# Performance work log

Measured on AMD Instinct MI355X. Metric: run time of the kernel, lower is better.

The kernel has to match this reference:

```python
import jax, jax.numpy as jnp
import numpy as np

VOCAB, E, H, B, T = 32000, 256, 512, 64, 512
PAD = VOCAB - 1


def setup_inputs() -> dict:
    key = jax.random.key(0)
    ks = jax.random.split(key, 9)
    s_ih = 1.0 / np.sqrt(H)
    inp = {
        "x": jax.random.randint(ks[0], (B, T), 0, VOCAB, dtype=jnp.int64 if jax.config.jax_enable_x64 else jnp.int32),
        "length": jax.random.randint(ks[1], (B, 1), 1, T + 1, dtype=jnp.int32),
        "embed_table": (jax.random.normal(ks[2], (VOCAB, E), dtype=jnp.float32)).at[PAD].set(0.0),
        "W_ih": jax.random.uniform(ks[3], (4 * H, E), jnp.float32, -s_ih, s_ih),
        "W_hh": jax.random.uniform(ks[4], (4 * H, H), jnp.float32, -s_ih, s_ih),
        "b_ih": jax.random.uniform(ks[5], (4 * H,), jnp.float32, -s_ih, s_ih),
        "b_hh": jax.random.uniform(ks[6], (4 * H,), jnp.float32, -s_ih, s_ih),
        "W_cls": jax.random.uniform(ks[7], (2, H), jnp.float32, -s_ih, s_ih),
        "b_cls": jax.random.uniform(ks[8], (2,), jnp.float32, -s_ih, s_ih),
    }
    return inp


def _lstm(xg, W_hh):
    # xg: [T, B, 4H] precomputed input-side gate activations; PyTorch gate order i,f,g,o
    Bn = xg.shape[1]
    h0 = jnp.zeros((Bn, H), xg.dtype)
    c0 = jnp.zeros((Bn, H), xg.dtype)

    def step(carry, g_in):
        h, c = carry
        g = g_in + h @ W_hh.T
        i, f, gg, o = jnp.split(g, 4, axis=-1)
        c = jax.nn.sigmoid(f) * c + jax.nn.sigmoid(i) * jnp.tanh(gg)
        h = jax.nn.sigmoid(o) * jnp.tanh(c)
        return (h, c), h

    _, hs = jax.lax.scan(step, (h0, c0), xg)
    return hs  # [T, B, H]


def reference(x, length, embed_table, W_ih, W_hh, b_ih, b_hh, W_cls, b_cls):
    emb_tab = embed_table.at[PAD].set(0.0)  # padding_idx row is zero
    we = emb_tab[x]  # [B, T, E]
    xg = jnp.einsum("bte,ge->btg", we, W_ih) + b_ih + b_hh  # [B, T, 4H]
    hs = _lstm(jnp.swapaxes(xg, 0, 1), W_hh)  # [T, B, H]
    hs = jnp.swapaxes(hs, 0, 1)  # [B, T, H]
    # ragged max-pool over valid timesteps
    mask = jnp.arange(T)[None, :] < length  # [B, T]
    neg = jnp.finfo(hs.dtype).min
    feature = jnp.max(jnp.where(mask[:, :, None], hs, neg), axis=1)  # [B, H]
    return feature @ W_cls.T + b_cls
```

## Files before the change

kernel.cpp:

```cpp
#include <hip/hip_runtime.h>
#include <hip/hip_bf16.h>

#define EN 256
#define HN 512
#define BN 64
#define TN 512
#define NBLK 64
#define KCAT 1280
#define NBUF 8
#define SLOTB 65536

typedef __attribute__((ext_vector_type(8))) short short8;
typedef __attribute__((ext_vector_type(4))) short short4v;
typedef __attribute__((ext_vector_type(4))) float f32x4;

#define SCOPE __HIP_MEMORY_SCOPE_AGENT
#define MFMA(A, B, C) __builtin_amdgcn_mfma_f32_16x16x32_bf16((A), (B), (C), 0, 0, 0)

__device__ inline short bf_of(float f) {
  __hip_bfloat16 h = __float2bfloat16(f);
  return *reinterpret_cast<short*>(&h);
}
__device__ inline float f_of_bf(short s) {
  __hip_bfloat16 h = *reinterpret_cast<__hip_bfloat16*>(&s);
  return __bfloat162float(h);
}

__global__ __launch_bounds__(256) void zero_kernel(unsigned* hb_u32,
                                                   unsigned* flags) {
  int idx = blockIdx.x * 256 + threadIdx.x;
  if (idx < SLOTB / 4)
    __hip_atomic_store(&hb_u32[idx], 0u, __ATOMIC_RELAXED, SCOPE);
  if (idx < NBLK)
    __hip_atomic_store(&flags[idx], 0u, __ATOMIC_RELAXED, SCOPE);
}

__global__ __launch_bounds__(256) void gather_kernel(
    short* __restrict__ weB, const int* __restrict__ x,
    const float* __restrict__ emb) {
  const int t = blockIdx.x;
  const int tid = threadIdx.x;
  const int b = tid >> 2, q = tid & 3;
  const int row = x[b * TN + t];
  const float4* src = (const float4*)(emb + (size_t)row * EN + q * 64);
  short* dst = weB + ((size_t)(t * 64 + b)) * EN + q * 64;
#pragma unroll
  for (int i = 0; i < 16; i++) {
    float4 v = src[i];
    short4v o = { bf_of(v.x), bf_of(v.y), bf_of(v.z), bf_of(v.w) };
    *(short4v*)(dst + i * 4) = o;
  }
}

__global__ __launch_bounds__(256) void prep_w_kernel(
    short* __restrict__ Wall, const float* __restrict__ Wih,
    const float* __restrict__ Whh) {
  int idx = blockIdx.x * 256 + threadIdx.x;
  int grow = idx / KCAT, kc = idx - grow * KCAT;
  float v;
  if (kc < 256) {
    v = Wih[(size_t)grow * EN + kc];
  } else if (kc < 768) {
    v = Whh[(size_t)grow * HN + (kc - 256)];
  } else {
    float f = Whh[(size_t)grow * HN + (kc - 768)];
    v = f - f_of_bf(bf_of(f));
  }
  Wall[idx] = bf_of(v);
}

__device__ __forceinline__ void poll_flags(const unsigned* flags,
                                           unsigned want, int l) {
  bool done = false;
  while (true) {
    if (!done) {
      unsigned v = __hip_atomic_load(&flags[l], __ATOMIC_RELAXED, SCOPE);
      done = (v >= want);
    }
    if (__all(done ? 1 : 0)) break;
    __builtin_amdgcn_s_sleep(1);
  }
  asm volatile("" ::: "memory");
}

#define HLOAD16_ISSUE                                                       \
  asm volatile(                                                             \
    "global_load_dwordx4 %0,  %16, off sc1\n\t"                             \
    "global_load_dwordx4 %1,  %16, off offset:1024 sc1\n\t"                 \
    "global_load_dwordx4 %2,  %16, off offset:2048 sc1\n\t"                 \
    "global_load_dwordx4 %3,  %16, off offset:3072 sc1\n\t"                 \
    "global_load_dwordx4 %4,  %17, off sc1\n\t"                             \
    "global_load_dwordx4 %5,  %17, off offset:1024 sc1\n\t"                 \
    "global_load_dwordx4 %6,  %17, off offset:2048 sc1\n\t"                 \
    "global_load_dwordx4 %7,  %17, off offset:3072 sc1\n\t"                 \
    "global_load_dwordx4 %8,  %18, off sc1\n\t"                             \
    "global_load_dwordx4 %9,  %18, off offset:1024 sc1\n\t"                 \
    "global_load_dwordx4 %10, %18, off offset:2048 sc1\n\t"                 \
    "global_load_dwordx4 %11, %18, off offset:3072 sc1\n\t"                 \
    "global_load_dwordx4 %12, %19, off sc1\n\t"                             \
    "global_load_dwordx4 %13, %19, off offset:1024 sc1\n\t"                 \
    "global_load_dwordx4 %14, %19, off offset:2048 sc1\n\t"                 \
    "global_load_dwordx4 %15, %19, off offset:3072 sc1"                     \
    : "=&v"(hv0), "=&v"(hv1), "=&v"(hv2),  "=&v"(hv3),                      \
      "=&v"(hv4), "=&v"(hv5), "=&v"(hv6),  "=&v"(hv7),                      \
      "=&v"(hv8), "=&v"(hv9), "=&v"(hv10), "=&v"(hv11),                     \
      "=&v"(hv12), "=&v"(hv13), "=&v"(hv14), "=&v"(hv15)                    \
    : "v"(hb0), "v"(hb1), "v"(hb2), "v"(hb3) : "memory")

#define WAIT_HALF                                                           \
  do {                                                                      \
    asm volatile("s_waitcnt vmcnt(8)"                                       \
                 : "+v"(hv0), "+v"(hv1), "+v"(hv2), "+v"(hv3),              \
                   "+v"(hv4), "+v"(hv5), "+v"(hv6), "+v"(hv7)               \
                 :: "memory");                                              \
    __builtin_amdgcn_sched_barrier(0);                                      \
  } while (0)

#define WAIT_ALL                                                            \
  do {                                                                      \
    asm volatile("s_waitcnt vmcnt(0)"                                       \
                 : "+v"(hv8), "+v"(hv9), "+v"(hv10), "+v"(hv11),            \
                   "+v"(hv12), "+v"(hv13), "+v"(hv14), "+v"(hv15)           \
                 :: "memory");                                              \
    __builtin_amdgcn_sched_barrier(0);                                      \
  } while (0)

__global__ __launch_bounds__(512, 1) void scan_kernel(
    const short* __restrict__ weB, const short* __restrict__ Wall,
    char* __restrict__ hb, const int* __restrict__ length,
    const float* __restrict__ bih, const float* __restrict__ bhh,
    const float* __restrict__ Wcls, const float* __restrict__ bcls,
    float* __restrict__ part, unsigned* flags, float* __restrict__ out) {
  __shared__ float gl[32][65];
  __shared__ __align__(16) short hstage[BN][8];
  const int tid = threadIdx.x;
  const int l = tid & 63, w = tid >> 6;
  const int bid = blockIdx.x;
  const int j0 = bid * 8;

  const int btile = (w & 3) * 16;
  const int rhalf = (w >> 2) * 16;

  short8 aH[24], aL[16];
  {
    int r = rhalf + (l & 15);
    int grow = (r >> 3) * HN + j0 + (r & 7);
    const short* wp = Wall + (size_t)grow * KCAT + 8 * (l >> 4);
#pragma unroll
    for (int kk = 0; kk < 24; kk++) aH[kk] = *(const short8*)(wp + kk * 32);
#pragma unroll
    for (int kk = 0; kk < 16; kk++) aL[kk] = *(const short8*)(wp + 768 + kk * 32);
  }

  const int jj = w, b = l;
  float bias[4];
#pragma unroll
  for (int ty = 0; ty < 4; ty++) {
    int grow = ty * HN + j0 + jj;
    bias[ty] = bih[grow] + bhh[grow];
  }
  const int len = length[b];
  float c = 0.f, fmx = -INFINITY;

  const int cons_off = (l >> 4) * 16384 + (btile + (l & 15)) * 16;
  const int prod_off = (bid & 3) * 16384 + (bid >> 2) * 1024 + l * 16;

  for (int t = 0; t < TN; t++) {
    const short* xrow = weB + ((size_t)(t * 64 + btile + (l & 15))) * EN + 8 * (l >> 4);
    short8 xf[8];
#pragma unroll
    for (int kk = 0; kk < 8; kk++) xf[kk] = *(const short8*)(xrow + kk * 32);
    f32x4 accH = {0.f, 0.f, 0.f, 0.f}, accL = {0.f, 0.f, 0.f, 0.f};
#pragma unroll
    for (int kk = 0; kk < 8; kk++)
      accH = MFMA(aH[kk], xf[kk], accH);

    if (w == 0) poll_flags(flags, (unsigned)t, l);
    __syncthreads();

    const char* hb0 = hb + (size_t)(t & 7) * SLOTB + cons_off;
    const char* hb1 = hb0 + 4096;
    const char* hb2 = hb0 + 8192;
    const char* hb3 = hb0 + 12288;
    short8 hv0, hv1, hv2, hv3, hv4, hv5, hv6, hv7;
    short8 hv8, hv9, hv10, hv11, hv12, hv13, hv14, hv15;
    HLOAD16_ISSUE;
    WAIT_HALF;
    accH = MFMA(aH[8],  hv0,  accH);  accL = MFMA(aL[0],  hv0,  accL);
    accH = MFMA(aH[9],  hv1,  accH);  accL = MFMA(aL[1],  hv1,  accL);
    accH = MFMA(aH[10], hv2,  accH);  accL = MFMA(aL[2],  hv2,  accL);
    accH = MFMA(aH[11], hv3,  accH);  accL = MFMA(aL[3],  hv3,  accL);
    accH = MFMA(aH[12], hv4,  accH);  accL = MFMA(aL[4],  hv4,  accL);
    accH = MFMA(aH[13], hv5,  accH);  accL = MFMA(aL[5],  hv5,  accL);
    accH = MFMA(aH[14], hv6,  accH);  accL = MFMA(aL[6],  hv6,  accL);
    accH = MFMA(aH[15], hv7,  accH);  accL = MFMA(aL[7],  hv7,  accL);
    WAIT_ALL;
    accH = MFMA(aH[16], hv8,  accH);  accL = MFMA(aL[8],  hv8,  accL);
    accH = MFMA(aH[17], hv9,  accH);  accL = MFMA(aL[9],  hv9,  accL);
    accH = MFMA(aH[18], hv10, accH);  accL = MFMA(aL[10], hv10, accL);
    accH = MFMA(aH[19], hv11, accH);  accL = MFMA(aL[11], hv11, accL);
    accH = MFMA(aH[20], hv12, accH);  accL = MFMA(aL[12], hv12, accL);
    accH = MFMA(aH[21], hv13, accH);  accL = MFMA(aL[13], hv13, accL);
    accH = MFMA(aH[22], hv14, accH);  accL = MFMA(aL[14], hv14, accL);
    accH = MFMA(aH[23], hv15, accH);  accL = MFMA(aL[15], hv15, accL);

#pragma unroll
    for (int q = 0; q < 4; q++) {
      int r = rhalf + (l >> 4) * 4 + q;
      gl[r][btile + (l & 15)] = accH[q] + accL[q];
    }
    __syncthreads();
    {
      float gi = gl[0 + jj][b] + bias[0];
      float gf = gl[8 + jj][b] + bias[1];
      float gg = gl[16 + jj][b] + bias[2];
      float go = gl[24 + jj][b] + bias[3];
      float si = 1.f / (1.f + __expf(-gi));
      float sf = 1.f / (1.f + __expf(-gf));
      float so = 1.f / (1.f + __expf(-go));
      float tg = 2.f / (1.f + __expf(-2.f * gg)) - 1.f;
      c = sf * c + si * tg;
      float tc = 2.f / (1.f + __expf(-2.f * c)) - 1.f;
      float h = so * tc;
      hstage[b][jj] = bf_of(h);
      if (t < len) fmx = fmaxf(fmx, h);
    }
    __syncthreads();
    if (w == 0) {
      short8 val = *(const short8*)&hstage[l][0];
      char* dp = hb + (size_t)((t + 1) & 7) * SLOTB + prod_off;
      asm volatile("global_store_dwordx4 %0, %1, off sc1"
                   :: "v"(dp), "v"(val) : "memory");
      asm volatile("s_waitcnt vmcnt(0)" ::: "memory");
      if (l == 0)
        __hip_atomic_store(&flags[bid], (unsigned)(t + 1),
                           __ATOMIC_RELAXED, SCOPE);
    }
  }

  gl[jj][b]      = fmx * Wcls[j0 + jj];
  gl[8 + jj][b]  = fmx * Wcls[HN + j0 + jj];
  __syncthreads();
  if (tid < 128) {
    int cls = tid >> 6, bb = tid & 63;
    float s = 0.f;
#pragma unroll
    for (int q = 0; q < 8; q++) s += gl[cls * 8 + q][bb];
    __hip_atomic_store(&part[(size_t)bid * 128 + cls * 64 + bb], s,
                       __ATOMIC_RELAXED, SCOPE);
  }
  __syncthreads();
  asm volatile("s_waitcnt vmcnt(0)" ::: "memory");
  if (tid == 0)
    __hip_atomic_store(&flags[bid], (unsigned)(TN + 1), __ATOMIC_RELAXED, SCOPE);
  if (bid == 0) {
    if (w == 0) poll_flags(flags, (unsigned)(TN + 1), l);
    __syncthreads();
    if (tid < 128) {
      int cls = tid >> 6, bb = tid & 63;
      float s = bcls[cls];
#pragma unroll 8
      for (int k = 0; k < NBLK; k++)
        s += __uint_as_float(__hip_atomic_load(
            (const unsigned*)&part[(size_t)k * 128 + cls * 64 + bb],
            __ATOMIC_RELAXED, SCOPE));
      out[bb * 2 + cls] = s;
    }
  }
}

extern "C" void kernel_launch(void* const* d_in, const int* in_sizes, int n_in,
                              void* d_out, int out_size, void* d_ws, size_t ws_size,
                              hipStream_t stream) {
  const int*   x    = (const int*)d_in[0];
  const int*   len  = (const int*)d_in[1];
  const float* emb  = (const float*)d_in[2];
  const float* Wih  = (const float*)d_in[3];
  const float* Whh  = (const float*)d_in[4];
  const float* bih  = (const float*)d_in[5];
  const float* bhh  = (const float*)d_in[6];
  const float* Wcls = (const float*)d_in[7];
  const float* bcls = (const float*)d_in[8];
  float* out = (float*)d_out;

  char* ws = (char*)d_ws;
  short* weB  = (short*)ws;
  short* Wall = (short*)(ws + 16777216ull);
  char*  hb   = ws + 16777216ull + 5242880;
  float* part = (float*)(ws + 16777216ull + 5242880 + 524288);
  unsigned* flagp = (unsigned*)(ws + 16777216ull + 5242880 + 524288 + 32768);

  zero_kernel<<<dim3(64), dim3(256), 0, stream>>>((unsigned*)hb, flagp);
  gather_kernel<<<dim3(TN), dim3(256), 0, stream>>>(weB, x, emb);
  prep_w_kernel<<<dim3((2048 * KCAT) / 256), dim3(256), 0, stream>>>(Wall, Wih, Whh);

  void* args[] = { (void*)&weB, (void*)&Wall, (void*)&hb, (void*)&len,
                   (void*)&bih, (void*)&bhh, (void*)&Wcls, (void*)&bcls,
                   (void*)&part, (void*)&flagp, (void*)&out };
  hipLaunchCooperativeKernel((void*)scan_kernel, dim3(NBLK), dim3(512),
                             args, 0, stream);
}
```

Before: 2.351 ms.

## Compute LSTM cell update in a single wave to drop a block barrier

The pointwise gate/cell update moves from all 8 waves (one hidden unit each) into wave 0, which loops over the 8 hidden units per batch lane and writes the bf16 h vector straight to global memory. This removes the hstage LDS staging and one __syncthreads per timestep on the serial recurrence. Flag polling moves to wave 7 and skips the block's own flag. The cost is 8x more serialized transcendental work in one wave on the critical path.

Result: slower. 3.550 ms (+51.0%).

```diff
diff --git a/kernel.cpp b/kernel.cpp
--- a/kernel.cpp
+++ b/kernel.cpp
@@ -70,8 +70,8 @@
 }
 
 __device__ __forceinline__ void poll_flags(const unsigned* flags,
-                                           unsigned want, int l) {
-  bool done = false;
+                                           unsigned want, int l, int bid) {
+  bool done = (l == bid);
   while (true) {
     if (!done) {
       unsigned v = __hip_atomic_load(&flags[l], __ATOMIC_RELAXED, SCOPE);
@@ -132,7 +132,7 @@
     const float* __restrict__ Wcls, const float* __restrict__ bcls,
     float* __restrict__ part, unsigned* flags, float* __restrict__ out) {
   __shared__ float gl[32][65];
-  __shared__ __align__(16) short hstage[BN][8];
+  __shared__ float bias_lds[32];
   const int tid = threadIdx.x;
   const int l = tid & 63, w = tid >> 6;
   const int bid = blockIdx.x;
@@ -152,15 +152,18 @@
     for (int kk = 0; kk < 16; kk++) aL[kk] = *(const short8*)(wp + 768 + kk * 32);
   }
 
-  const int jj = w, b = l;
-  float bias[4];
-#pragma unroll
-  for (int ty = 0; ty < 4; ty++) {
-    int grow = ty * HN + j0 + jj;
-    bias[ty] = bih[grow] + bhh[grow];
-  }
-  const int len = length[b];
-  float c = 0.f, fmx = -INFINITY;
+  if (tid < 32) {
+    int grow = (tid >> 3) * HN + j0 + (tid & 7);
+    bias_lds[tid] = bih[grow] + bhh[grow];
+  }
+
+  float c8[8] = {0.f, 0.f, 0.f, 0.f, 0.f, 0.f, 0.f, 0.f};
+  float fmx8[8];
+#pragma unroll
+  for (int i = 0; i < 8; i++) fmx8[i] = -INFINITY;
+  int len0 = 0;
+  if (w == 0) len0 = length[l];
+  __syncthreads();
 
   const int cons_off = (l >> 4) * 16384 + (btile + (l & 15)) * 16;
   const int prod_off = (bid & 3) * 16384 + (bid >> 2) * 1024 + l * 16;
@@ -175,7 +178,7 @@
     for (int kk = 0; kk < 8; kk++)
       accH = MFMA(aH[kk], xf[kk], accH);
 
-    if (w == 0) poll_flags(flags, (unsigned)t, l);
+    if (w == 7) poll_flags(flags, (unsigned)t, l, bid);
     __syncthreads();
 
     const char* hb0 = hb + (size_t)(t & 7) * SLOTB + cons_off;
@@ -210,24 +213,25 @@
       gl[r][btile + (l & 15)] = accH[q] + accL[q];
     }
     __syncthreads();
-    {
-      float gi = gl[0 + jj][b] + bias[0];
-      float gf = gl[8 + jj][b] + bias[1];
-      float gg = gl[16 + jj][b] + bias[2];
-      float go = gl[24 + jj][b] + bias[3];
-      float si = 1.f / (1.f + __expf(-gi));
-      float sf = 1.f / (1.f + __expf(-gf));
-      float so = 1.f / (1.f + __expf(-go));
-      float tg = 2.f / (1.f + __expf(-2.f * gg)) - 1.f;
-      c = sf * c + si * tg;
-      float tc = 2.f / (1.f + __expf(-2.f * c)) - 1.f;
-      float h = so * tc;
-      hstage[b][jj] = bf_of(h);
-      if (t < len) fmx = fmaxf(fmx, h);
-    }
-    __syncthreads();
+
     if (w == 0) {
-      short8 val = *(const short8*)&hstage[l][0];
+      short8 val;
+#pragma unroll
+      for (int jj = 0; jj < 8; jj++) {
+        float gi = gl[jj][l]      + bias_lds[jj];
+        float gf = gl[8 + jj][l]  + bias_lds[8 + jj];
+        float gg = gl[16 + jj][l] + bias_lds[16 + jj];
+        float go = gl[24 + jj][l] + bias_lds[24 + jj];
+        float si = 1.f / (1.f + __expf(-gi));
+        float sf = 1.f / (1.f + __expf(-gf));
+        float so = 1.f / (1.f + __expf(-go));
+        float tg = 2.f / (1.f + __expf(-2.f * gg)) - 1.f;
+        c8[jj] = sf * c8[jj] + si * tg;
+        float tc = 2.f / (1.f + __expf(-2.f * c8[jj])) - 1.f;
+        float h = so * tc;
+        val[jj] = bf_of(h);
+        if (t < len0) fmx8[jj] = fmaxf(fmx8[jj], h);
+      }
       char* dp = hb + (size_t)((t + 1) & 7) * SLOTB + prod_off;
       asm volatile("global_store_dwordx4 %0, %1, off sc1"
                    :: "v"(dp), "v"(val) : "memory");
@@ -238,23 +242,25 @@
     }
   }
 
-  gl[jj][b]      = fmx * Wcls[j0 + jj];
-  gl[8 + jj][b]  = fmx * Wcls[HN + j0 + jj];
-  __syncthreads();
-  if (tid < 128) {
-    int cls = tid >> 6, bb = tid & 63;
-    float s = 0.f;
-#pragma unroll
-    for (int q = 0; q < 8; q++) s += gl[cls * 8 + q][bb];
-    __hip_atomic_store(&part[(size_t)bid * 128 + cls * 64 + bb], s,
-                       __ATOMIC_RELAXED, SCOPE);
-  }
-  __syncthreads();
-  asm volatile("s_waitcnt vmcnt(0)" ::: "memory");
-  if (tid == 0)
-    __hip_atomic_store(&flags[bid], (unsigned)(TN + 1), __ATOMIC_RELAXED, SCOPE);
+  if (w == 0) {
+    float s0 = 0.f, s1 = 0.f;
+#pragma unroll
+    for (int jj = 0; jj < 8; jj++) {
+      s0 += fmx8[jj] * Wcls[j0 + jj];
+      s1 += fmx8[jj] * Wcls[HN + j0 + jj];
+    }
+    __hip_atomic_store((unsigned*)&part[(size_t)bid * 128 + l],
+                       __float_as_uint(s0), __ATOMIC_RELAXED, SCOPE);
+    __hip_atomic_store((unsigned*)&part[(size_t)bid * 128 + 64 + l],
+                       __float_as_uint(s1), __ATOMIC_RELAXED, SCOPE);
+    asm volatile("s_waitcnt vmcnt(0)" ::: "memory");
+    if (l == 0)
+      __hip_atomic_store(&flags[bid], (unsigned)(TN + 1),
+                         __ATOMIC_RELAXED, SCOPE);
+  }
   if (bid == 0) {
-    if (w == 0) poll_flags(flags, (unsigned)(TN + 1), l);
+    __syncthreads();
+    if (w == 0) poll_flags(flags, (unsigned)(TN + 1), l, bid);
     __syncthreads();
     if (tid < 128) {
       int cls = tid >> 6, bb = tid & 63;
```
